# Kernel optimization log

Measured on AMD Instinct MI355X. Metric: run time of the kernel, lower is better.

The kernel has to match this reference:

```python
import jax, jax.numpy as jnp
import numpy as np

K = 9            # base neighbors
MAX_DILATION = 3


def setup_inputs() -> dict:
    key = jax.random.key(0)
    x = jax.random.normal(key, (64, 256, 1024), dtype=jnp.float32)  # (B, C, N)
    return {"x": x, "layer_idx": 8}


def reference(x, layer_idx):
    # x: (B, C, N); layer_idx: python int
    B, C, N = x.shape
    dilation = min(layer_idx // 4 + 1, MAX_DILATION)
    k_d = K * dilation

    pts = jnp.transpose(x, (0, 2, 1))  # (B, N, C) points per graph segment
    # squared euclidean pairwise distances (same neighbor ordering as euclidean)
    sq = jnp.sum(pts * pts, axis=-1)                       # (B, N)
    d2 = sq[:, :, None] + sq[:, None, :] \
         - 2.0 * jnp.einsum('bnc,bmc->bnm', pts, pts)      # (B, N, N)

    # k_d nearest neighbors of each node (self included, as in DGL bruteforce knn)
    _, idx = jax.lax.top_k(-d2, k_d)                       # (B, N, k_d)

    # segmented graph: offset node ids per batch element
    offs = (jnp.arange(B) * N)[:, None, None]
    src = (idx + offs).reshape(-1)                         # neighbor -> node edges
    dst = jnp.repeat(jnp.arange(B * N), k_d)

    # dilation: take every `dilation`-th edge; since k_d = K*dilation and each
    # node's edges are contiguous, every node keeps exactly K edges
    src_d = src[::dilation]
    dst_d = dst[::dilation]
    # eval mode: no stochastic edge dropout; include_self=False -> no added self loops
    return src_d, dst_d
```

## Files before the change

kernel.cpp:

```cpp
#include <hip/hip_runtime.h>


typedef __bf16 bf16x8 __attribute__((ext_vector_type(8)));
typedef float  f32x4  __attribute__((ext_vector_type(4)));
typedef unsigned int u32;

#define B_   64
#define C_   256
#define N_   1024
#define NSRC (B_ * N_ * 9)

#define STRIDE_I 1088
#define BUFB     17408

__device__ __forceinline__ u32 umin_(u32 a, u32 b) { return a < b ? a : b; }
__device__ __forceinline__ u32 umax_(u32 a, u32 b) { return a > b ? a : b; }

__device__ __forceinline__ void load_lds16(const void* g, void* l) {
    __builtin_amdgcn_global_load_lds((const __attribute__((address_space(1))) void*)g,
                                     (__attribute__((address_space(3))) void*)l,
                                     16, 0, 0);
}

__global__ __launch_bounds__(256, 4) void trans_kernel(const float* __restrict__ X,
                                                       unsigned short* __restrict__ XT,
                                                       float* __restrict__ NRM) {
    __shared__ u32 T2[128][66];
    const int tid = threadIdx.x;
    const int b   = blockIdx.x >> 4;
    const int n0  = (blockIdx.x & 15) * 64;

    {
        const int cpl = tid >> 4;
        const int s   = tid & 15;
#pragma unroll
        for (int it = 0; it < 8; ++it) {
            const int c0 = it * 32 + cpl * 2;
            const float* src = X + ((size_t)b * C_ + c0) * N_ + n0 + s * 4;
            float4 f0 = *(const float4*)(src);
            float4 f1 = *(const float4*)(src + N_);
            const float a0[4] = {f0.x, f0.y, f0.z, f0.w};
            const float a1[4] = {f1.x, f1.y, f1.z, f1.w};
            u32 pk[4];
#pragma unroll
            for (int j = 0; j < 4; ++j) {
                u32 u0 = __float_as_uint(a0[j]);
                u32 u1 = __float_as_uint(a1[j]);
                u32 b0 = (u0 + 0x7FFFu + ((u0 >> 16) & 1u)) >> 16;
                u32 b1 = (u1 + 0x7FFFu + ((u1 >> 16) & 1u)) >> 16;
                pk[j] = b0 | (b1 << 16);
            }
            *(uint4*)&T2[it * 16 + cpl][s * 4] = make_uint4(pk[0], pk[1], pk[2], pk[3]);
        }
    }
    __syncthreads();

    {
        const int rr = tid >> 2, p = tid & 3;
        unsigned short* xtrow = XT + ((size_t)b * N_ + n0 + rr) * C_;
        float nsq = 0.f;
#pragma unroll
        for (int j = 0; j < 8; ++j) {
            u32 x0 = T2[j * 16 + 4 * p + 0][rr];
            u32 x1 = T2[j * 16 + 4 * p + 1][rr];
            u32 x2 = T2[j * 16 + 4 * p + 2][rr];
            u32 x3 = T2[j * 16 + 4 * p + 3][rr];
            const u32 xs[4] = {x0, x1, x2, x3};
#pragma unroll
            for (int q = 0; q < 4; ++q) {
                float lo = __uint_as_float(xs[q] << 16);
                float hi = __uint_as_float(xs[q] & 0xFFFF0000u);
                nsq = fmaf(lo, lo, fmaf(hi, hi, nsq));
            }
            *(uint4*)((char*)xtrow + j * 64 + p * 16) = make_uint4(x0, x1, x2, x3);
        }
        nsq += __shfl_xor(nsq, 1);
        nsq += __shfl_xor(nsq, 2);
        if (p == 0) NRM[b * N_ + n0 + rr] = nsq + 512.0f;
    }
}

#define SORT8(v)                                                              \
    do {                                                                      \
        u32 mn, mx;                                                           \
        mn = umin_(v[0], v[4]); mx = umax_(v[0], v[4]); v[0] = mn; v[4] = mx; \
        mn = umin_(v[1], v[5]); mx = umax_(v[1], v[5]); v[1] = mn; v[5] = mx; \
        mn = umin_(v[2], v[6]); mx = umax_(v[2], v[6]); v[2] = mn; v[6] = mx; \
        mn = umin_(v[3], v[7]); mx = umax_(v[3], v[7]); v[3] = mn; v[7] = mx; \
        mn = umin_(v[0], v[2]); mx = umax_(v[0], v[2]); v[0] = mn; v[2] = mx; \
        mn = umin_(v[1], v[3]); mx = umax_(v[1], v[3]); v[1] = mn; v[3] = mx; \
        mn = umin_(v[4], v[6]); mx = umax_(v[4], v[6]); v[4] = mn; v[6] = mx; \
        mn = umin_(v[5], v[7]); mx = umax_(v[5], v[7]); v[5] = mn; v[7] = mx; \
        mn = umin_(v[0], v[1]); mx = umax_(v[0], v[1]); v[0] = mn; v[1] = mx; \
        mn = umin_(v[2], v[3]); mx = umax_(v[2], v[3]); v[2] = mn; v[3] = mx; \
        mn = umin_(v[4], v[5]); mx = umax_(v[4], v[5]); v[4] = mn; v[5] = mx; \
        mn = umin_(v[6], v[7]); mx = umax_(v[6], v[7]); v[6] = mn; v[7] = mx; \
    } while (0)

__global__ __launch_bounds__(256, 4) void knn_mfma_kernel(const unsigned short* __restrict__ XT,
                                                          const float* __restrict__ NRM,
                                                          int* __restrict__ out) {
    __shared__ __align__(1024) char Bt[2 * BUFB];

    const int tid  = threadIdx.x;
    const int lane = tid & 63;
    const int w    = tid >> 6;

    const int bi = blockIdx.x;
    const int b  = (bi & 7) + 8 * (bi >> 7);
    const int n0 = ((bi >> 3) & 15) * 64;

    const int lrow = lane & 15;
    const int g    = lane >> 4;
    const bool odd = lane & 1;
    const bool hiP = (lane >> 1) & 1;

    const unsigned short* xtb = XT + (size_t)b * N_ * C_;
    const float* nrmb = NRM + b * N_;

    bf16x8 afr[8];
    {
        const unsigned short* ap = xtb + (n0 + w * 16 + lrow) * C_ + g * 8;
#pragma unroll
        for (int kc = 0; kc < 8; ++kc)
            afr[kc] = *(const bf16x8*)(ap + kc * 32);
    }

    u32 L[4][6];
#pragma unroll
    for (int r = 0; r < 4; ++r)
#pragma unroll
        for (int i = 0; i < 6; ++i) L[r][i] = 0xFFFFFFFFu;

    const int lh   = lane >> 5;
    const int col0 = (lane & 31) * 16;

    {
        const char* gb = (const char*)(xtb + (size_t)(w * 8) * C_);
        char* ldsw = Bt + (w * 4) * STRIDE_I;
#pragma unroll
        for (int i = 0; i < 4; ++i) {
            const int rt  = i * 2 + lh;
            const int col = (col0 - (((w * 8 + rt) & 15) * 16)) & 511;
            load_lds16(gb + (size_t)rt * 512 + col, ldsw + i * STRIDE_I);
        }
    }
    __syncthreads();

#pragma unroll 1
    for (int c = 0; c < 32; ++c) {
        const float nm0 = nrmb[c * 32 + lrow];
        const float nm1 = nrmb[c * 32 + 16 + lrow];

        if (c < 31) {
            const int cn = c + 1;
            const char* gb = (const char*)(xtb + (size_t)(cn * 32 + w * 8) * C_);
            char* ldsw = Bt + (cn & 1) * BUFB + (w * 4) * STRIDE_I;
#pragma unroll
            for (int i = 0; i < 4; ++i) {
                const int rt  = i * 2 + lh;
                const int col = (col0 - (((w * 8 + rt) & 15) * 16)) & 511;
                load_lds16(gb + (size_t)rt * 512 + col, ldsw + i * STRIDE_I);
            }
        }

        const char* bufc = Bt + (c & 1) * BUFB;
#pragma unroll
        for (int t = 0; t < 2; ++t) {
            const char* rbase = bufc + t * 8704 + (lrow >> 1) * STRIDE_I + (lrow & 1) * 512;
            f32x4 acc = {0.f, 0.f, 0.f, 0.f};
#pragma unroll
            for (int kc = 0; kc < 8; ++kc) {
                bf16x8 bfr = *(const bf16x8*)(rbase + ((kc * 64 + g * 16 + lrow * 16) & 511));
                acc = __builtin_amdgcn_mfma_f32_16x16x32_bf16(afr[kc], bfr, acc, 0, 0, 0);
            }
            const int m = c * 32 + t * 16 + lrow;
            const float nm = t ? nm1 : nm0;
#pragma unroll
            for (int r = 0; r < 4; ++r) {
                float f = fmaf(-2.f, acc[r], nm);
                u32 u = __float_as_uint(f);
                u32 cur = (u & 0xFFFFFC00u) | (u32)m;
                u32 p0 = L[r][0], p1 = L[r][1], p2 = L[r][2];
                u32 p3 = L[r][3], p4 = L[r][4], p5 = L[r][5];
                L[r][0] = umin_(p0, cur);
                L[r][1] = umax_(p0, umin_(p1, cur));
                L[r][2] = umax_(p1, umin_(p2, cur));
                L[r][3] = umax_(p2, umin_(p3, cur));
                L[r][4] = umax_(p3, umin_(p4, cur));
                L[r][5] = umax_(p4, umin_(p5, cur));
            }
        }
        __syncthreads();
    }

    int* out_src = out;
    int* out_dst = out + NSRC;
#pragma unroll
    for (int r = 0; r < 4; ++r) {
        u32 v[8], t1[8];
#pragma unroll
        for (int i = 0; i < 6; ++i) v[i] = L[r][i];
        v[6] = 0xFFFFFFFFu; v[7] = 0xFFFFFFFFu;

#pragma unroll
        for (int i = 0; i < 8; ++i) t1[i] = __shfl_xor(v[i], 1);
#pragma unroll
        for (int i = 0; i < 8; ++i) {
            u32 mn = umin_(v[i], t1[7 - i]);
            u32 mx = umax_(v[i], t1[7 - i]);
            v[i] = odd ? mx : mn;
        }
        SORT8(v);

#pragma unroll
        for (int i = 0; i < 8; ++i) t1[i] = __shfl_xor(v[i], 3);
#pragma unroll
        for (int i = 0; i < 8; ++i) {
            u32 mn = umin_(v[i], t1[7 - i]);
            u32 mx = umax_(v[i], t1[7 - i]);
            v[i] = hiP ? mx : mn;
        }
#pragma unroll
        for (int i = 0; i < 8; ++i) t1[i] = __shfl_xor(v[i], 1);
#pragma unroll
        for (int i = 0; i < 8; ++i)
            v[i] = odd ? umax_(v[i], t1[i]) : umin_(v[i], t1[i]);
        SORT8(v);

#pragma unroll
        for (int s = 0; s < 2; ++s) {
            const int mask = s ? 11 : 7;
#pragma unroll
            for (int i = 0; i < 8; ++i) t1[i] = __shfl_xor(v[i], mask);
#pragma unroll
            for (int i = 0; i < 8; ++i) v[i] = umin_(v[i], t1[7 - i]);
#pragma unroll
            for (int i = 0; i < 8; ++i) t1[i] = __shfl_xor(v[i], 2);
#pragma unroll
            for (int i = 0; i < 8; ++i)
                v[i] = hiP ? umax_(v[i], t1[i]) : umin_(v[i], t1[i]);
#pragma unroll
            for (int i = 0; i < 8; ++i) t1[i] = __shfl_xor(v[i], 1);
#pragma unroll
            for (int i = 0; i < 8; ++i)
                v[i] = odd ? umax_(v[i], t1[i]) : umin_(v[i], t1[i]);
            SORT8(v);
        }

        if ((lane & 12) == 0) {
            const int rank0 = (hiP ? 16 : 0) + (odd ? 8 : 0);
            const int obase = (b * N_ + n0 + w * 16 + 4 * g + r) * 9;
#pragma unroll
            for (int i = 0; i < 8; ++i) {
                const int rank = rank0 + i;
                if (rank < 25 && (rank % 3) == 0)
                    out_src[obase + rank / 3] = (b << 10) | (int)(v[i] & 1023u);
            }
        }
    }

    const int jbase = (b * N_ + n0) * 9;
    for (int idx = tid; idx < 576; idx += 256)
        out_dst[jbase + idx] = (jbase + idx) / 9;
}

__global__ __launch_bounds__(256, 2) void knn_kernel(const float* __restrict__ X,
                                                     int* __restrict__ out) {
    __shared__ float smem[16 * N_];
    const int tid = threadIdx.x;
    const int b  = blockIdx.x >> 6;
    const int n0 = (blockIdx.x & 63) * 16;
    const float* __restrict__ xb = X + (size_t)b * C_ * N_;
#pragma unroll
    for (int i = 0; i < 16; ++i) {
        int f = tid + i * 256;
        int c = f >> 4, qq = f & 15;
        smem[f] = xb[c * N_ + n0 + qq];
    }
    __syncthreads();
    float acc[16][4];
#pragma unroll
    for (int q = 0; q < 16; ++q) { acc[q][0] = acc[q][1] = acc[q][2] = acc[q][3] = 0.f; }
    float nrm[4] = {0.f, 0.f, 0.f, 0.f};
    for (int c = 0; c < C_; ++c) {
        const float* __restrict__ xc = xb + c * N_;
        float bv0 = xc[tid], bv1 = xc[tid + 256], bv2 = xc[tid + 512], bv3 = xc[tid + 768];
        const float4* A4 = reinterpret_cast<const float4*>(smem + c * 16);
        float4 a0 = A4[0], a1 = A4[1], a2 = A4[2], a3 = A4[3];
        float aq[16] = {a0.x, a0.y, a0.z, a0.w, a1.x, a1.y, a1.z, a1.w,
                        a2.x, a2.y, a2.z, a2.w, a3.x, a3.y, a3.z, a3.w};
#pragma unroll
        for (int q = 0; q < 16; ++q) {
            acc[q][0] = fmaf(aq[q], bv0, acc[q][0]);
            acc[q][1] = fmaf(aq[q], bv1, acc[q][1]);
            acc[q][2] = fmaf(aq[q], bv2, acc[q][2]);
            acc[q][3] = fmaf(aq[q], bv3, acc[q][3]);
        }
        nrm[0] = fmaf(bv0, bv0, nrm[0]); nrm[1] = fmaf(bv1, bv1, nrm[1]);
        nrm[2] = fmaf(bv2, bv2, nrm[2]); nrm[3] = fmaf(bv3, bv3, nrm[3]);
    }
    __syncthreads();
#pragma unroll
    for (int q = 0; q < 16; ++q) {
        smem[q * N_ + tid]       = nrm[0] - 2.f * acc[q][0];
        smem[q * N_ + tid + 256] = nrm[1] - 2.f * acc[q][1];
        smem[q * N_ + tid + 512] = nrm[2] - 2.f * acc[q][2];
        smem[q * N_ + tid + 768] = nrm[3] - 2.f * acc[q][3];
    }
    __syncthreads();
    const int lane = tid & 63;
    const int w    = tid >> 6;
    int* out_src = out;
    int* out_dst = out + NSRC;
    for (int q = w; q < 16; q += 4) {
        float v[16];
#pragma unroll
        for (int i = 0; i < 16; ++i) v[i] = smem[q * N_ + lane + i * 64];
        float lv = v[0]; int ls = 0;
#pragma unroll
        for (int i = 1; i < 16; ++i) { if (v[i] < lv) { lv = v[i]; ls = i; } }
        int lm = lane + (ls << 6);
        const int obase = (b * N_ + n0 + q) * 9;
#pragma unroll
        for (int r = 0; r < 25; ++r) {
            float bv = lv; int bm = lm;
#pragma unroll
            for (int off = 32; off >= 1; off >>= 1) {
                float ov = __shfl_xor(bv, off);
                int   om = __shfl_xor(bm, off);
                if (ov < bv || (ov == bv && om < bm)) { bv = ov; bm = om; }
            }
            if ((r % 3) == 0 && lane == 0) out_src[obase + r / 3] = b * N_ + bm;
            if (bm == lm) {
#pragma unroll
                for (int i = 0; i < 16; ++i) { if (i == ls) v[i] = 3.4e38f; }
                lv = v[0]; ls = 0;
#pragma unroll
                for (int i = 1; i < 16; ++i) { if (v[i] < lv) { lv = v[i]; ls = i; } }
                lm = lane + (ls << 6);
            }
        }
    }
    const int jbase = (b * N_ + n0) * 9;
    if (tid < 16 * 9) out_dst[jbase + tid] = (jbase + tid) / 9;
}

extern "C" void kernel_launch(void* const* d_in, const int* in_sizes, int n_in,
                              void* d_out, int out_size, void* d_ws, size_t ws_size,
                              hipStream_t stream) {
    (void)in_sizes; (void)n_in; (void)out_size;
    const float* X = (const float*)d_in[0];
    int* out = (int*)d_out;
    const size_t xt_bytes  = (size_t)B_ * N_ * C_ * 2;
    const size_t nrm_bytes = (size_t)B_ * N_ * 4;
    if (ws_size >= xt_bytes + nrm_bytes) {
        unsigned short* XT = (unsigned short*)d_ws;
        float* NRM = (float*)((char*)d_ws + xt_bytes);
        trans_kernel<<<dim3(B_ * 16), dim3(256), 0, stream>>>(X, XT, NRM);
        knn_mfma_kernel<<<dim3(B_ * 16), dim3(256), 0, stream>>>(XT, NRM, out);
    } else {
        knn_kernel<<<dim3(B_ * 64), dim3(256), 0, stream>>>(X, out);
    }
}
```

Baseline: 169.5 us.

## Retile transpose kernel by channel chunks and accumulate norms with fixed-point atomics

The transpose kernel now tiles each block as 64 channels by 256 points instead of all 256 channels by 64 points. Global reads become 1 KB contiguous row segments, which should give better coalescing. Because each block now sees only part of the channels, the squared norms are built as fixed-point integer atomicAdds into a buffer zeroed by an added memset. The knn kernel converts these back to float. This adds a memset launch and atomic traffic, and the fixed-point norm quantization could slightly perturb neighbor ordering.

```diff
diff --git a/kernel.cpp b/kernel.cpp
--- a/kernel.cpp
+++ b/kernel.cpp
@@ -11,7 +11,7 @@
 #define NSRC (B_ * N_ * 9)
 
 #define STRIDE_I 1088
-#define BUFB     17408
+#define REGION_W 8704
 
 __device__ __forceinline__ u32 umin_(u32 a, u32 b) { return a < b ? a : b; }
 __device__ __forceinline__ u32 umax_(u32 a, u32 b) { return a > b ? a : b; }
@@ -24,59 +24,64 @@
 
 __global__ __launch_bounds__(256, 4) void trans_kernel(const float* __restrict__ X,
                                                        unsigned short* __restrict__ XT,
-                                                       float* __restrict__ NRM) {
-    __shared__ u32 T2[128][66];
+                                                       u32* __restrict__ NRMU) {
+    __shared__ u32 T2[32][257];
     const int tid = threadIdx.x;
-    const int b   = blockIdx.x >> 4;
-    const int n0  = (blockIdx.x & 15) * 64;
+    const int bi  = blockIdx.x;
+    const int b   = bi >> 4;
+    const int c0  = ((bi >> 2) & 3) * 64;
+    const int n0  = (bi & 3) * 256;
+    const int w   = tid >> 6;
+    const int l   = tid & 63;
 
     {
-        const int cpl = tid >> 4;
-        const int s   = tid & 15;
-#pragma unroll
-        for (int it = 0; it < 8; ++it) {
-            const int c0 = it * 32 + cpl * 2;
-            const float* src = X + ((size_t)b * C_ + c0) * N_ + n0 + s * 4;
+        const int n4 = l * 4;
+#pragma unroll
+        for (int i = 0; i < 8; ++i) {
+            const int rp = i * 4 + w;
+            const float* src = X + ((size_t)(b * C_ + c0 + 2 * rp)) * N_ + n0 + n4;
             float4 f0 = *(const float4*)(src);
             float4 f1 = *(const float4*)(src + N_);
             const float a0[4] = {f0.x, f0.y, f0.z, f0.w};
             const float a1[4] = {f1.x, f1.y, f1.z, f1.w};
-            u32 pk[4];
 #pragma unroll
             for (int j = 0; j < 4; ++j) {
                 u32 u0 = __float_as_uint(a0[j]);
                 u32 u1 = __float_as_uint(a1[j]);
                 u32 b0 = (u0 + 0x7FFFu + ((u0 >> 16) & 1u)) >> 16;
                 u32 b1 = (u1 + 0x7FFFu + ((u1 >> 16) & 1u)) >> 16;
-                pk[j] = b0 | (b1 << 16);
-            }
-            *(uint4*)&T2[it * 16 + cpl][s * 4] = make_uint4(pk[0], pk[1], pk[2], pk[3]);
+                T2[rp][n4 + j] = b0 | (b1 << 16);
+            }
         }
     }
     __syncthreads();
 
     {
-        const int rr = tid >> 2, p = tid & 3;
-        unsigned short* xtrow = XT + ((size_t)b * N_ + n0 + rr) * C_;
-        float nsq = 0.f;
-#pragma unroll
-        for (int j = 0; j < 8; ++j) {
-            u32 x0 = T2[j * 16 + 4 * p + 0][rr];
-            u32 x1 = T2[j * 16 + 4 * p + 1][rr];
-            u32 x2 = T2[j * 16 + 4 * p + 2][rr];
-            u32 x3 = T2[j * 16 + 4 * p + 3][rr];
+        const int k  = tid & 7;
+        const int nB = tid >> 3;
+#pragma unroll
+        for (int nn = 0; nn < 8; ++nn) {
+            const int n = nn * 32 + nB;
+            u32 x0 = T2[4 * k + 0][n];
+            u32 x1 = T2[4 * k + 1][n];
+            u32 x2 = T2[4 * k + 2][n];
+            u32 x3 = T2[4 * k + 3][n];
             const u32 xs[4] = {x0, x1, x2, x3};
+            float ps = 0.f;
 #pragma unroll
             for (int q = 0; q < 4; ++q) {
                 float lo = __uint_as_float(xs[q] << 16);
                 float hi = __uint_as_float(xs[q] & 0xFFFF0000u);
-                nsq = fmaf(lo, lo, fmaf(hi, hi, nsq));
-            }
-            *(uint4*)((char*)xtrow + j * 64 + p * 16) = make_uint4(x0, x1, x2, x3);
-        }
-        nsq += __shfl_xor(nsq, 1);
-        nsq += __shfl_xor(nsq, 2);
-        if (p == 0) NRM[b * N_ + n0 + rr] = nsq + 512.0f;
+                ps = fmaf(lo, lo, fmaf(hi, hi, ps));
+            }
+            *(uint4*)((char*)XT + ((size_t)(b * N_ + n0 + n)) * 512 + c0 * 2 + k * 16) =
+                make_uint4(x0, x1, x2, x3);
+            ps += __shfl_xor(ps, 1);
+            ps += __shfl_xor(ps, 2);
+            ps += __shfl_xor(ps, 4);
+            if (k == 0)
+                atomicAdd(NRMU + b * N_ + n0 + n, (u32)(ps * 1048576.0f + 0.5f));
+        }
     }
 }
 
@@ -98,9 +103,9 @@
     } while (0)
 
 __global__ __launch_bounds__(256, 4) void knn_mfma_kernel(const unsigned short* __restrict__ XT,
-                                                          const float* __restrict__ NRM,
+                                                          const u32* __restrict__ NRMU,
                                                           int* __restrict__ out) {
-    __shared__ __align__(1024) char Bt[2 * BUFB];
+    __shared__ __align__(1024) char Bt[2 * 17408];
 
     const int tid  = threadIdx.x;
     const int lane = tid & 63;
@@ -116,7 +121,7 @@
     const bool hiP = (lane >> 1) & 1;
 
     const unsigned short* xtb = XT + (size_t)b * N_ * C_;
-    const float* nrmb = NRM + b * N_;
+    const u32* nrmb = NRMU + b * N_;
 
     bf16x8 afr[8];
     {
@@ -149,13 +154,15 @@
 
 #pragma unroll 1
     for (int c = 0; c < 32; ++c) {
-        const float nm0 = nrmb[c * 32 + lrow];
-        const float nm1 = nrmb[c * 32 + 16 + lrow];
+        const u32 nu0 = nrmb[c * 32 + lrow];
+        const u32 nu1 = nrmb[c * 32 + 16 + lrow];
+        const float nm0 = fmaf((float)nu0, 0x1p-20f, 512.0f);
+        const float nm1 = fmaf((float)nu1, 0x1p-20f, 512.0f);
 
         if (c < 31) {
             const int cn = c + 1;
             const char* gb = (const char*)(xtb + (size_t)(cn * 32 + w * 8) * C_);
-            char* ldsw = Bt + (cn & 1) * BUFB + (w * 4) * STRIDE_I;
+            char* ldsw = Bt + (cn & 1) * 17408 + (w * 4) * STRIDE_I;
 #pragma unroll
             for (int i = 0; i < 4; ++i) {
                 const int rt  = i * 2 + lh;
@@ -164,7 +171,7 @@
             }
         }
 
-        const char* bufc = Bt + (c & 1) * BUFB;
+        const char* bufc = Bt + (c & 1) * 17408;
 #pragma unroll
         for (int t = 0; t < 2; ++t) {
             const char* rbase = bufc + t * 8704 + (lrow >> 1) * STRIDE_I + (lrow & 1) * 512;
@@ -356,9 +363,10 @@
     const size_t nrm_bytes = (size_t)B_ * N_ * 4;
     if (ws_size >= xt_bytes + nrm_bytes) {
         unsigned short* XT = (unsigned short*)d_ws;
-        float* NRM = (float*)((char*)d_ws + xt_bytes);
-        trans_kernel<<<dim3(B_ * 16), dim3(256), 0, stream>>>(X, XT, NRM);
-        knn_mfma_kernel<<<dim3(B_ * 16), dim3(256), 0, stream>>>(XT, NRM, out);
+        u32* NRMU = (u32*)((char*)d_ws + xt_bytes);
+        hipMemsetAsync(NRMU, 0, nrm_bytes, stream);
+        trans_kernel<<<dim3(B_ * 16), dim3(256), 0, stream>>>(X, XT, NRMU);
+        knn_mfma_kernel<<<dim3(B_ * 16), dim3(256), 0, stream>>>(XT, NRMU, out);
     } else {
         knn_kernel<<<dim3(B_ * 64), dim3(256), 0, stream>>>(X, out);
     }
```

After: 169.9 us. About the same (+0.2%).
